# Kernel tuning notes

Measured on AMD Instinct MI355X. Metric: run time of the kernel, lower is better.

## Reference

```python
import jax, jax.numpy as jnp
import numpy as np

TAU_PLUS = 0.1
BETA = 1.0
TEMPERATURE = 0.5
EPS = 1e-8


def setup_inputs() -> dict:
    key = jax.random.key(0)
    B = 4096
    logits = jax.random.normal(key, (B, B), dtype=jnp.float32)
    return {"logits": logits}


def reference(logits):
    B = logits.shape[0]
    t = TEMPERATURE
    N = 2 * B - 2

    # positive pairs: diagonal twice
    d = jnp.diagonal(logits)
    pos = jnp.exp(jnp.concatenate([d, d]) / t)  # [2B]

    # 2B x 2B block similarity matrix [[L, L^T], [L^T, L]]
    sim = jnp.block([[logits, logits.T], [logits.T, logits]])

    # analytic negative mask: exclude diagonal and the paired entry (|i-j| == B)
    idx = jnp.arange(2 * B)
    diff = jnp.abs(idx[:, None] - idx[None, :])
    mask = (diff != 0) & (diff != B)  # [2B, 2B] bool, N true per row

    neg = jnp.where(mask, jnp.exp(sim / t), 0.0)  # masked entries contribute 0

    # hard-negative reweighting: imp = exp(beta * log(neg)) = neg**beta on kept entries
    safe_neg = jnp.where(mask, neg, 1.0)  # avoid log(0)
    imp = jnp.where(mask, jnp.exp(BETA * jnp.log(safe_neg)), 0.0)
    # torch mean over N kept columns == sum / N
    reweight_neg = (imp * neg).sum(axis=1) / (imp.sum(axis=1) / N)

    Ng = (-TAU_PLUS * N * pos + reweight_neg) / (1.0 - TAU_PLUS)
    Ng = jnp.maximum(Ng, N * jnp.exp(jnp.asarray(-1.0 / t, dtype=logits.dtype)))

    loss = -jnp.log(pos / (pos + Ng + EPS))
    return loss.mean()
```

## Files before the change

### kernel.cpp

```cpp
#include <hip/hip_runtime.h>
#include <math.h>


#define THREADS    256
#define TILE_ROWS  16
#define EXP_SCALE  2.885390081777927f

__global__ __launch_bounds__(THREADS) void pass1_kernel(
    const float* __restrict__ L,
    float* __restrict__ rowE,
    float* __restrict__ rowE2,
    float* __restrict__ colPE,
    float* __restrict__ colPE2,
    int B)
{
    __shared__ float2 rp[TILE_ROWS][THREADS];

    const int t       = threadIdx.x;
    const int colBase = blockIdx.x * (THREADS * 4) + 4 * t;
    const int s       = blockIdx.y;
    const int row0    = s * TILE_ROWS;

    float c0 = 0.f, c1 = 0.f, c2 = 0.f, c3 = 0.f;
    float d0 = 0.f, d1 = 0.f, d2 = 0.f, d3 = 0.f;

#pragma unroll
    for (int r = 0; r < TILE_ROWS; ++r) {
        const float4 x = *reinterpret_cast<const float4*>(
            L + (size_t)(row0 + r) * B + colBase);
        float e0 = exp2f(x.x * EXP_SCALE);
        float e1 = exp2f(x.y * EXP_SCALE);
        float e2 = exp2f(x.z * EXP_SCALE);
        float e3 = exp2f(x.w * EXP_SCALE);
        float q0 = e0 * e0, q1 = e1 * e1, q2 = e2 * e2, q3 = e3 * e3;
        c0 += e0; c1 += e1; c2 += e2; c3 += e3;
        d0 += q0; d1 += q1; d2 += q2; d3 += q3;
        rp[r][t] = make_float2((e0 + e1) + (e2 + e3), (q0 + q1) + (q2 + q3));
    }
    __syncthreads();

    const int wave = t >> 6;
    const int lane = t & 63;
#pragma unroll
    for (int r = wave; r < TILE_ROWS; r += 4) {
        float2 a = rp[r][lane];
        float2 b = rp[r][lane + 64];
        float2 c = rp[r][lane + 128];
        float2 d = rp[r][lane + 192];
        float se  = (a.x + b.x) + (c.x + d.x);
        float se2 = (a.y + b.y) + (c.y + d.y);
#pragma unroll
        for (int off = 32; off > 0; off >>= 1) {
            se  += __shfl_down(se,  off, 64);
            se2 += __shfl_down(se2, off, 64);
        }
        if (lane == 0) {
            atomicAdd(&rowE [row0 + r], se);
            atomicAdd(&rowE2[row0 + r], se2);
        }
    }

    *reinterpret_cast<float4*>(colPE  + (size_t)s * B + colBase) = make_float4(c0, c1, c2, c3);
    *reinterpret_cast<float4*>(colPE2 + (size_t)s * B + colBase) = make_float4(d0, d1, d2, d3);
}

__global__ __launch_bounds__(THREADS) void pass2_kernel(
    const float* __restrict__ L,
    const float* __restrict__ rowE,
    const float* __restrict__ rowE2,
    const float* __restrict__ colPE,
    const float* __restrict__ colPE2,
    float* __restrict__ out,
    int B, int S)
{
    const int t    = threadIdx.x;
    const int c    = t & 15;
    const int g    = t >> 4;
    const int base = blockIdx.x * 16;

    float se = 0.f, se2 = 0.f;
    for (int k = g; k < S; k += 16) {
        se  += colPE [(size_t)k * B + base + c];
        se2 += colPE2[(size_t)k * B + base + c];
    }
    __shared__ float2 part[16][17];
    part[g][c] = make_float2(se, se2);
    __syncthreads();

    if (t < 16) {
        float colE = 0.f, colE2 = 0.f;
#pragma unroll
        for (int gg = 0; gg < 16; ++gg) {
            colE  += part[gg][t].x;
            colE2 += part[gg][t].y;
        }
        const int i  = base + t;
        const float Nf = (float)(2 * B - 2);
        float dg = L[(size_t)i * B + i];
        float pe = exp2f(dg * EXP_SCALE);
        float S1 = rowE [i] + colE  - 2.f * pe;
        float S2 = rowE2[i] + colE2 - 2.f * (pe * pe);
        float rw = Nf * (S2 / S1);
        float Ng = (rw - 0.1f * Nf * pe) * (1.f / 0.9f);
        Ng = fmaxf(Ng, Nf * 0.13533528323661270f);
        float loss = logf((pe + Ng + 1e-8f) / pe);
#pragma unroll
        for (int off = 8; off > 0; off >>= 1) loss += __shfl_down(loss, off, 16);
        if (t == 0) atomicAdd(out, loss / (float)B);
    }
}

extern "C" void kernel_launch(void* const* d_in, const int* in_sizes, int n_in,
                              void* d_out, int out_size, void* d_ws, size_t ws_size,
                              hipStream_t stream) {
    const float* L = (const float*)d_in[0];
    int B = 1;
    while ((long long)B * B < (long long)in_sizes[0]) B <<= 1;
    const int S = B / TILE_ROWS;

    float* rowE   = (float*)d_ws;
    float* rowE2  = rowE  + B;
    float* colPE  = rowE2 + B;
    float* colPE2 = colPE + (size_t)S * B;

    hipMemsetAsync(d_ws, 0, (size_t)2 * B * sizeof(float), stream);
    hipMemsetAsync(d_out, 0, sizeof(float), stream);

    dim3 grid1(B / (THREADS * 4), B / TILE_ROWS);
    pass1_kernel<<<grid1, THREADS, 0, stream>>>(L, rowE, rowE2, colPE, colPE2, B);
    pass2_kernel<<<B / 16, THREADS, 0, stream>>>(L, rowE, rowE2, colPE, colPE2,
                                                 (float*)d_out, B, S);
}
```

Before: 103.3 us.

## Use per-wave row stripes with row partial buffers instead of LDS and atomics

Pass 1 now assigns each wave its own stripe of 4 rows by 1024 columns. Row sums are reduced entirely within the wave using shuffles and written to per-column-block partial buffers, which removes the shared-memory tile, the block barrier, the row atomics and the workspace memset. Pass 2 is rebuilt so each block handles 64 columns, with 4 waves splitting the stripe reduction, and it sums the 4 row partials itself. The trade-off is that column partials grow from B/16 to B/4 stripes. That quadruples the intermediate traffic written by pass 1 and read by pass 2, and it needs a larger workspace.

```diff
diff --git a/kernel.cpp b/kernel.cpp
--- a/kernel.cpp
+++ b/kernel.cpp
@@ -3,110 +3,112 @@
 
 
 #define THREADS    256
-#define TILE_ROWS  16
 #define EXP_SCALE  2.885390081777927f
 
 __global__ __launch_bounds__(THREADS) void pass1_kernel(
     const float* __restrict__ L,
-    float* __restrict__ rowE,
-    float* __restrict__ rowE2,
+    float* __restrict__ rowPE,
+    float* __restrict__ rowPE2,
     float* __restrict__ colPE,
     float* __restrict__ colPE2,
     int B)
 {
-    __shared__ float2 rp[TILE_ROWS][THREADS];
+    const int lane    = threadIdx.x & 63;
+    const int wave    = threadIdx.x >> 6;
+    const int x       = blockIdx.x;
+    const int stripe  = blockIdx.y * 4 + wave;
+    const int row0    = stripe * 4;
+    const int colBase = x * 1024 + lane * 4;
 
-    const int t       = threadIdx.x;
-    const int colBase = blockIdx.x * (THREADS * 4) + 4 * t;
-    const int s       = blockIdx.y;
-    const int row0    = s * TILE_ROWS;
-
-    float c0 = 0.f, c1 = 0.f, c2 = 0.f, c3 = 0.f;
-    float d0 = 0.f, d1 = 0.f, d2 = 0.f, d3 = 0.f;
+    float cE[16], cE2[16];
+#pragma unroll
+    for (int k = 0; k < 16; ++k) { cE[k] = 0.f; cE2[k] = 0.f; }
 
 #pragma unroll
-    for (int r = 0; r < TILE_ROWS; ++r) {
-        const float4 x = *reinterpret_cast<const float4*>(
-            L + (size_t)(row0 + r) * B + colBase);
-        float e0 = exp2f(x.x * EXP_SCALE);
-        float e1 = exp2f(x.y * EXP_SCALE);
-        float e2 = exp2f(x.z * EXP_SCALE);
-        float e3 = exp2f(x.w * EXP_SCALE);
-        float q0 = e0 * e0, q1 = e1 * e1, q2 = e2 * e2, q3 = e3 * e3;
-        c0 += e0; c1 += e1; c2 += e2; c3 += e3;
-        d0 += q0; d1 += q1; d2 += q2; d3 += q3;
-        rp[r][t] = make_float2((e0 + e1) + (e2 + e3), (q0 + q1) + (q2 + q3));
-    }
-    __syncthreads();
-
-    const int wave = t >> 6;
-    const int lane = t & 63;
+    for (int r = 0; r < 4; ++r) {
+        const float* Lr = L + (size_t)(row0 + r) * B + colBase;
+        float rs = 0.f, rs2 = 0.f;
 #pragma unroll
-    for (int r = wave; r < TILE_ROWS; r += 4) {
-        float2 a = rp[r][lane];
-        float2 b = rp[r][lane + 64];
-        float2 c = rp[r][lane + 128];
-        float2 d = rp[r][lane + 192];
-        float se  = (a.x + b.x) + (c.x + d.x);
-        float se2 = (a.y + b.y) + (c.y + d.y);
+        for (int j = 0; j < 4; ++j) {
+            const float4 v = *reinterpret_cast<const float4*>(Lr + j * 256);
+            float e0 = exp2f(v.x * EXP_SCALE);
+            float e1 = exp2f(v.y * EXP_SCALE);
+            float e2 = exp2f(v.z * EXP_SCALE);
+            float e3 = exp2f(v.w * EXP_SCALE);
+            float q0 = e0 * e0, q1 = e1 * e1, q2 = e2 * e2, q3 = e3 * e3;
+            cE [j * 4 + 0] += e0; cE [j * 4 + 1] += e1;
+            cE [j * 4 + 2] += e2; cE [j * 4 + 3] += e3;
+            cE2[j * 4 + 0] += q0; cE2[j * 4 + 1] += q1;
+            cE2[j * 4 + 2] += q2; cE2[j * 4 + 3] += q3;
+            rs  += (e0 + e1) + (e2 + e3);
+            rs2 += (q0 + q1) + (q2 + q3);
+        }
 #pragma unroll
         for (int off = 32; off > 0; off >>= 1) {
-            se  += __shfl_down(se,  off, 64);
-            se2 += __shfl_down(se2, off, 64);
+            rs  += __shfl_down(rs,  off, 64);
+            rs2 += __shfl_down(rs2, off, 64);
         }
         if (lane == 0) {
-            atomicAdd(&rowE [row0 + r], se);
-            atomicAdd(&rowE2[row0 + r], se2);
+            rowPE [(size_t)x * B + row0 + r] = rs;
+            rowPE2[(size_t)x * B + row0 + r] = rs2;
         }
     }
 
-    *reinterpret_cast<float4*>(colPE  + (size_t)s * B + colBase) = make_float4(c0, c1, c2, c3);
-    *reinterpret_cast<float4*>(colPE2 + (size_t)s * B + colBase) = make_float4(d0, d1, d2, d3);
+    float* cpe  = colPE  + (size_t)stripe * B + colBase;
+    float* cpe2 = colPE2 + (size_t)stripe * B + colBase;
+#pragma unroll
+    for (int j = 0; j < 4; ++j) {
+        *reinterpret_cast<float4*>(cpe  + j * 256) =
+            make_float4(cE [j*4+0], cE [j*4+1], cE [j*4+2], cE [j*4+3]);
+        *reinterpret_cast<float4*>(cpe2 + j * 256) =
+            make_float4(cE2[j*4+0], cE2[j*4+1], cE2[j*4+2], cE2[j*4+3]);
+    }
 }
 
 __global__ __launch_bounds__(THREADS) void pass2_kernel(
     const float* __restrict__ L,
-    const float* __restrict__ rowE,
-    const float* __restrict__ rowE2,
+    const float* __restrict__ rowPE,
+    const float* __restrict__ rowPE2,
     const float* __restrict__ colPE,
     const float* __restrict__ colPE2,
     float* __restrict__ out,
     int B, int S)
 {
     const int t    = threadIdx.x;
-    const int c    = t & 15;
-    const int g    = t >> 4;
-    const int base = blockIdx.x * 16;
+    const int lane = t & 63;
+    const int wave = t >> 6;
+    const int col  = blockIdx.x * 64 + lane;
 
     float se = 0.f, se2 = 0.f;
-    for (int k = g; k < S; k += 16) {
-        se  += colPE [(size_t)k * B + base + c];
-        se2 += colPE2[(size_t)k * B + base + c];
+    const int k0 = wave * (S / 4), k1 = k0 + (S / 4);
+#pragma unroll 8
+    for (int k = k0; k < k1; ++k) {
+        se  += colPE [(size_t)k * B + col];
+        se2 += colPE2[(size_t)k * B + col];
     }
-    __shared__ float2 part[16][17];
-    part[g][c] = make_float2(se, se2);
+    __shared__ float2 part[4][64];
+    part[wave][lane] = make_float2(se, se2);
     __syncthreads();
 
-    if (t < 16) {
-        float colE = 0.f, colE2 = 0.f;
-#pragma unroll
-        for (int gg = 0; gg < 16; ++gg) {
-            colE  += part[gg][t].x;
-            colE2 += part[gg][t].y;
-        }
-        const int i  = base + t;
+    if (wave == 0) {
+        float colE  = (part[0][lane].x + part[1][lane].x) + (part[2][lane].x + part[3][lane].x);
+        float colE2 = (part[0][lane].y + part[1][lane].y) + (part[2][lane].y + part[3][lane].y);
+        const int i = col;
+        float rowE  = (rowPE [i] + rowPE [B + i]) + (rowPE [2*B + i] + rowPE [3*B + i]);
+        float rowE2 = (rowPE2[i] + rowPE2[B + i]) + (rowPE2[2*B + i] + rowPE2[3*B + i]);
+
         const float Nf = (float)(2 * B - 2);
         float dg = L[(size_t)i * B + i];
         float pe = exp2f(dg * EXP_SCALE);
-        float S1 = rowE [i] + colE  - 2.f * pe;
-        float S2 = rowE2[i] + colE2 - 2.f * (pe * pe);
+        float S1 = rowE  + colE  - 2.f * pe;
+        float S2 = rowE2 + colE2 - 2.f * (pe * pe);
         float rw = Nf * (S2 / S1);
         float Ng = (rw - 0.1f * Nf * pe) * (1.f / 0.9f);
         Ng = fmaxf(Ng, Nf * 0.13533528323661270f);
         float loss = logf((pe + Ng + 1e-8f) / pe);
 #pragma unroll
-        for (int off = 8; off > 0; off >>= 1) loss += __shfl_down(loss, off, 16);
-        if (t == 0) atomicAdd(out, loss / (float)B);
+        for (int off = 32; off > 0; off >>= 1) loss += __shfl_down(loss, off, 64);
+        if (lane == 0) atomicAdd(out, loss / (float)B);
     }
 }
 
@@ -116,18 +118,17 @@
     const float* L = (const float*)d_in[0];
     int B = 1;
     while ((long long)B * B < (long long)in_sizes[0]) B <<= 1;
-    const int S = B / TILE_ROWS;
+    const int S = B / 4;
 
-    float* rowE   = (float*)d_ws;
-    float* rowE2  = rowE  + B;
-    float* colPE  = rowE2 + B;
-    float* colPE2 = colPE + (size_t)S * B;
+    float* rowPE  = (float*)d_ws;
+    float* rowPE2 = rowPE  + (size_t)4 * B;
+    float* colPE  = rowPE2 + (size_t)4 * B;
+    float* colPE2 = colPE  + (size_t)S * B;
 
-    hipMemsetAsync(d_ws, 0, (size_t)2 * B * sizeof(float), stream);
     hipMemsetAsync(d_out, 0, sizeof(float), stream);
 
-    dim3 grid1(B / (THREADS * 4), B / TILE_ROWS);
-    pass1_kernel<<<grid1, THREADS, 0, stream>>>(L, rowE, rowE2, colPE, colPE2, B);
-    pass2_kernel<<<B / 16, THREADS, 0, stream>>>(L, rowE, rowE2, colPE, colPE2,
+    dim3 grid1(4, B / 16);
+    pass1_kernel<<<grid1, THREADS, 0, stream>>>(L, rowPE, rowPE2, colPE, colPE2, B);
+    pass2_kernel<<<B / 64, THREADS, 0, stream>>>(L, rowPE, rowPE2, colPE, colPE2,
                                                  (float*)d_out, B, S);
 }
```

After: 111.3 us. 7.8% more time.
